# Kernel optimization log

Hardware: AMD Instinct MI355X
Metric: run time of the kernel (lower is better)

## Reference

```python
import jax, jax.numpy as jnp
import numpy as np

ALPHA = 0.2  # LeakyReLU negative slope


def setup_inputs() -> dict:
    key = jax.random.key(0)
    k1, k2, k3, k4 = jax.random.split(key, 4)
    N, IN, OUT = 8192, 512, 256
    x = jax.random.normal(k1, (N, IN), dtype=jnp.float32)
    adj = jnp.zeros((N, N), dtype=jnp.float32)  # accepted but unused by the module
    W = jax.random.normal(k2, (OUT, IN), dtype=jnp.float32) * (1.0 / np.sqrt(IN))
    a1 = jax.random.normal(k3, (OUT,), dtype=jnp.float32) * (1.0 / np.sqrt(OUT))
    a2 = jax.random.normal(k4, (OUT,), dtype=jnp.float32) * (1.0 / np.sqrt(OUT))
    return {"x": x, "adj": adj, "W": W, "a1": a1, "a2": a2}


def reference(x, adj, W, a1, a2):
    # h = tran(x): [N, OUT]
    h = x @ W.T
    # additive GAT scores: e[i, j] = a2 . h_i + a1 . h_j  (from unsqueeze(0)+unsqueeze(1))
    s1 = h @ a1  # [N], att1(h)
    s2 = h @ a2  # [N], att2(h)
    e = s2[:, None] + s1[None, :]  # [N, N]
    e = jnp.where(e > 0, e, ALPHA * e)  # LeakyReLU
    attn = jax.nn.softmax(e, axis=1)  # softmax over dim=1; dropout is identity in eval
    return attn @ h  # [N, OUT]
```

## Files before the change

### kernel.cpp

```cpp
#include <hip/hip_runtime.h>

#define NROW 8192
#define DIN  512
#define DOUT 256
#define NCHUNK 256
#define CLEN 32

constexpr size_t OFF_H      = 0;
constexpr size_t OFF_S1     = OFF_H + (size_t)NROW*DOUT*4;
constexpr size_t OFF_S2     = OFF_S1 + NROW*4;
constexpr size_t OFF_RANK   = OFF_S2 + NROW*4;
constexpr size_t OFF_MISC   = OFF_RANK + NROW*4;
constexpr size_t MEMSET_LEN = OFF_MISC + 256 - OFF_S1;
constexpr size_t OFF_S1S    = OFF_MISC + 256;
constexpr size_t OFF_PERM   = OFF_S1S + NROW*4;
constexpr size_t OFF_WHI    = OFF_PERM + NROW*4;
constexpr size_t OFF_WLO    = OFF_WHI + NROW*4;
constexpr size_t OFF_PRELOS = OFF_WLO + NROW*4;
constexpr size_t OFF_SUFHIS = OFF_PRELOS + 33024;
constexpr size_t OFF_CSLO   = OFF_SUFHIS + 33024;
constexpr size_t OFF_CSHI   = OFF_CSLO + 1024;
constexpr size_t OFF_TLO    = OFF_CSHI + 1024;
constexpr size_t OFF_THI    = OFF_TLO + (size_t)NCHUNK*DOUT*4;
constexpr size_t OFF_PRELO  = OFF_THI + (size_t)NCHUNK*DOUT*4;
constexpr size_t OFF_SUFHI  = OFF_PRELO + (size_t)(NROW+1)*DOUT*4;
constexpr size_t WS_NEED    = OFF_SUFHI + (size_t)(NROW+1)*DOUT*4;

typedef float f32x4 __attribute__((ext_vector_type(4)));
typedef short s16x8 __attribute__((ext_vector_type(8)));

__device__ __forceinline__ unsigned short bf16_rne(float f) {
  unsigned int u = __float_as_uint(f);
  return (unsigned short)((u + 0x7fffu + ((u >> 16) & 1u)) >> 16);
}
__device__ __forceinline__ unsigned short bf16_part(float f, bool lo) {
  unsigned short hi = bf16_rne(f);
  if (!lo) return hi;
  float r = f - __uint_as_float(((unsigned int)hi) << 16);
  return bf16_rne(r);
}
__device__ __forceinline__ s16x8 cvt8(const float4 u, const float4 v, bool lo) {
  s16x8 r;
  r[0] = (short)bf16_part(u.x, lo); r[1] = (short)bf16_part(u.y, lo);
  r[2] = (short)bf16_part(u.z, lo); r[3] = (short)bf16_part(u.w, lo);
  r[4] = (short)bf16_part(v.x, lo); r[5] = (short)bf16_part(v.y, lo);
  r[6] = (short)bf16_part(v.z, lo); r[7] = (short)bf16_part(v.w, lo);
  return r;
}

__global__ __launch_bounds__(256) void gemm_h_mfma(const float* __restrict__ x,
                                                   const float* __restrict__ W,
                                                   float* __restrict__ h) {
  __shared__ unsigned short As[64][40];
  __shared__ unsigned short Bs[64][40];
  const int tid = threadIdx.x;
  const int rowBase = blockIdx.x * 64;
  const int colBase = blockIdx.y * 64;
  const int wid = tid >> 6, lane = tid & 63;
  const int wRow = wid >> 1, wCol = wid & 1;
  const int lhi = lane >> 4, llo = lane & 15;

  f32x4 acc[2][2];
#pragma unroll
  for (int m = 0; m < 2; ++m)
#pragma unroll
    for (int n = 0; n < 2; ++n) acc[m][n] = (f32x4)(0.f);

  const int sr = tid >> 2;
  const int sq = tid & 3;
  const float* xsrc = x + (size_t)(rowBase + sr) * DIN + sq * 8;
  const float* wsrc = W + (size_t)(colBase + sr) * DIN + sq * 8;

  for (int pass = 0; pass < 3; ++pass) {
    const bool aLo = (pass == 1);
    const bool bLo = (pass == 2);
    for (int k0 = 0; k0 < DIN; k0 += 32) {
      float4 a0 = *(const float4*)(xsrc + k0);
      float4 a1v = *(const float4*)(xsrc + k0 + 4);
      float4 b0 = *(const float4*)(wsrc + k0);
      float4 b1 = *(const float4*)(wsrc + k0 + 4);
      s16x8 av = cvt8(a0, a1v, aLo);
      s16x8 bv = cvt8(b0, b1, bLo);
      __syncthreads();
      *(s16x8*)&As[sr][sq * 8] = av;
      *(s16x8*)&Bs[sr][sq * 8] = bv;
      __syncthreads();
      s16x8 af[2], bf[2];
#pragma unroll
      for (int m = 0; m < 2; ++m)
        af[m] = *(const s16x8*)&As[wRow * 32 + m * 16 + llo][lhi * 8];
#pragma unroll
      for (int n = 0; n < 2; ++n)
        bf[n] = *(const s16x8*)&Bs[wCol * 32 + n * 16 + llo][lhi * 8];
#pragma unroll
      for (int m = 0; m < 2; ++m)
#pragma unroll
        for (int n = 0; n < 2; ++n)
          acc[m][n] = __builtin_amdgcn_mfma_f32_16x16x32_bf16(af[m], bf[n], acc[m][n], 0, 0, 0);
    }
  }
#pragma unroll
  for (int m = 0; m < 2; ++m)
#pragma unroll
    for (int n = 0; n < 2; ++n) {
      const int col = colBase + wCol * 32 + n * 16 + llo;
#pragma unroll
      for (int j = 0; j < 4; ++j) {
        const int row = rowBase + wRow * 32 + m * 16 + lhi * 4 + j;
        h[(size_t)row * DOUT + col] = acc[m][n][j];
      }
    }
}

__global__ __launch_bounds__(256) void s1s2_rows(const float* __restrict__ h,
                                                 const float* __restrict__ a1,
                                                 const float* __restrict__ a2,
                                                 float* __restrict__ s1,
                                                 float* __restrict__ s2) {
  const int wid = threadIdx.x >> 6, lane = threadIdx.x & 63;
  const int row = blockIdx.x * 4 + wid;
  float4 hv = *(const float4*)(h + (size_t)row * DOUT + (lane << 2));
  float4 A1 = *(const float4*)(a1 + (lane << 2));
  float4 A2 = *(const float4*)(a2 + (lane << 2));
  float p1 = hv.x * A1.x + hv.y * A1.y + hv.z * A1.z + hv.w * A1.w;
  float p2 = hv.x * A2.x + hv.y * A2.y + hv.z * A2.z + hv.w * A2.w;
#pragma unroll
  for (int off = 32; off > 0; off >>= 1) {
    p1 += __shfl_xor(p1, off);
    p2 += __shfl_xor(p2, off);
  }
  if (lane == 0) { s1[row] = p1; s2[row] = p2; }
}

__global__ __launch_bounds__(256) void rank_count(const float* __restrict__ s1,
                                                  int* __restrict__ rank,
                                                  unsigned int* __restrict__ miscu) {
  __shared__ float sj[1024];
  __shared__ float wm[4];
  const int t = threadIdx.x;
  const int ib = blockIdx.x, jc = blockIdx.y;
  const int j0 = jc * 1024;
  *(float4*)&sj[t << 2] = *(const float4*)(s1 + j0 + (t << 2));
  const int i = ib * 256 + t;
  const float v = s1[i];
  __syncthreads();
  int cnt = 0;
#pragma unroll 4
  for (int q = 0; q < 256; ++q) {
    float4 sv = *(const float4*)&sj[q << 2];
    int jg = j0 + (q << 2);
    cnt += (int)(sv.x < v) + (int)((sv.x == v) & (jg + 0 < i));
    cnt += (int)(sv.y < v) + (int)((sv.y == v) & (jg + 1 < i));
    cnt += (int)(sv.z < v) + (int)((sv.z == v) & (jg + 2 < i));
    cnt += (int)(sv.w < v) + (int)((sv.w == v) & (jg + 3 < i));
  }
  atomicAdd(&rank[i], cnt);
  if (jc == 0) {
    float m = v;
#pragma unroll
    for (int off = 32; off > 0; off >>= 1) m = fmaxf(m, __shfl_down(m, off));
    if ((t & 63) == 0) wm[t >> 6] = m;
    __syncthreads();
    if (t == 0) {
      float mm = fmaxf(fmaxf(wm[0], wm[1]), fmaxf(wm[2], wm[3]));
      unsigned int b = __float_as_uint(mm);
      unsigned int enc = (b & 0x80000000u) ? ~b : (b | 0x80000000u);
      atomicMax(miscu, enc);
    }
  }
}

__global__ __launch_bounds__(256) void scatter_w(const float* __restrict__ s1,
                                                 const int* __restrict__ rank,
                                                 const unsigned int* __restrict__ miscu,
                                                 float* __restrict__ miscf,
                                                 float* __restrict__ s1s,
                                                 int* __restrict__ perm,
                                                 float* __restrict__ w_hi,
                                                 float* __restrict__ w_lo) {
  const int i = blockIdx.x * 256 + threadIdx.x;
  unsigned int e = miscu[0];
  unsigned int b = (e & 0x80000000u) ? (e & 0x7fffffffu) : ~e;
  const float M1 = __uint_as_float(b);
  const float v = s1[i];
  const int r = rank[i];
  s1s[r] = v;
  perm[r] = i;
  w_hi[r] = __expf(v - M1);
  w_lo[r] = __expf(0.2f * (v - M1));
  if (i == 0) miscf[0] = M1;
}

__global__ __launch_bounds__(256) void chunk_totals(const float* __restrict__ h,
                                                    const int* __restrict__ perm,
                                                    const float* __restrict__ w_hi,
                                                    const float* __restrict__ w_lo,
                                                    float* __restrict__ T_lo,
                                                    float* __restrict__ T_hi,
                                                    float* __restrict__ cs_lo,
                                                    float* __restrict__ cs_hi) {
  const int d = threadIdx.x, b = blockIdx.x;
  const int j0 = b * CLEN;
  float tlo = 0.f, thi = 0.f;
#pragma unroll
  for (int e = 0; e < CLEN; e += 4) {
    int4 p4 = *(const int4*)(perm + j0 + e);
    float4 wl4 = *(const float4*)(w_lo + j0 + e);
    float4 wh4 = *(const float4*)(w_hi + j0 + e);
    float h0 = h[(size_t)p4.x * DOUT + d];
    float h1 = h[(size_t)p4.y * DOUT + d];
    float h2 = h[(size_t)p4.z * DOUT + d];
    float h3 = h[(size_t)p4.w * DOUT + d];
    tlo += wl4.x * h0 + wl4.y * h1 + wl4.z * h2 + wl4.w * h3;
    thi += wh4.x * h0 + wh4.y * h1 + wh4.z * h2 + wh4.w * h3;
  }
  T_lo[b * DOUT + d] = tlo;
  T_hi[b * DOUT + d] = thi;
  if (d < 64) {
    float wl = (d < 32) ? w_lo[j0 + d] : 0.f;
    float wh = (d < 32) ? w_hi[j0 + d] : 0.f;
#pragma unroll
    for (int off = 32; off > 0; off >>= 1) {
      wl += __shfl_down(wl, off);
      wh += __shfl_down(wh, off);
    }
    if (d == 0) { cs_lo[b] = wl; cs_hi[b] = wh; }
  }
}

__global__ __launch_bounds__(256) void write_prefix(const float* __restrict__ h,
                                                    const int* __restrict__ perm,
                                                    const float* __restrict__ w_hi,
                                                    const float* __restrict__ w_lo,
                                                    const float* __restrict__ T_lo,
                                                    const float* __restrict__ T_hi,
                                                    const float* __restrict__ cs_lo,
                                                    const float* __restrict__ cs_hi,
                                                    float* __restrict__ PreLo,
                                                    float* __restrict__ SufHi,
                                                    float* __restrict__ prelo_s,
                                                    float* __restrict__ sufhi_s) {
  const int d = threadIdx.x, b = blockIdx.x;
  const int j0 = b * CLEN;
  if (d < 64) {
    float accp = 0.f, acct = 0.f;
    for (int p = d; p < NCHUNK; p += 64) {
      float cl = cs_lo[p], ch = cs_hi[p];
      accp += (p < b) ? cl : 0.f;
      acct += (p > b) ? ch : 0.f;
    }
#pragma unroll
    for (int off = 32; off > 0; off >>= 1) {
      accp += __shfl_down(accp, off);
      acct += __shfl_down(acct, off);
    }
    float pres  = __shfl(accp, 0);
    float tails = __shfl(acct, 0);
    float wl = (d < 32) ? w_lo[j0 + d] : 0.f;
    float wh = (d < 32) ? w_hi[j0 + d] : 0.f;
    float pl = wl, ph = wh;
#pragma unroll
    for (int off = 1; off < 32; off <<= 1) {
      float a = __shfl_up(pl, off);
      float c = __shfl_up(ph, off);
      if (d >= off) { pl += a; ph += c; }
    }
    float chunk_hi_tot = __shfl(ph, 31);
    if (d < 32) {
      prelo_s[j0 + d] = pres + (pl - wl);
      sufhi_s[j0 + d] = tails + (chunk_hi_tot - (ph - wh));
    }
    if (b == NCHUNK - 1 && d == 31) {
      prelo_s[NROW] = pres + pl;
      sufhi_s[NROW] = 0.f;
    }
  }
  float rl = 0.f, tail = 0.f;
#pragma unroll 8
  for (int p = 0; p < NCHUNK; ++p) {
    float vl = T_lo[p * DOUT + d];
    float vh = T_hi[p * DOUT + d];
    rl   += (p < b) ? vl : 0.f;
    tail += (p > b) ? vh : 0.f;
  }
  float hv[CLEN], wlv[CLEN], whv[CLEN];
  float ownHi = 0.f;
#pragma unroll
  for (int e = 0; e < CLEN; e += 4) {
    int4 p4 = *(const int4*)(perm + j0 + e);
    float4 wl4 = *(const float4*)(w_lo + j0 + e);
    float4 wh4 = *(const float4*)(w_hi + j0 + e);
    hv[e + 0] = h[(size_t)p4.x * DOUT + d];
    hv[e + 1] = h[(size_t)p4.y * DOUT + d];
    hv[e + 2] = h[(size_t)p4.z * DOUT + d];
    hv[e + 3] = h[(size_t)p4.w * DOUT + d];
    wlv[e + 0] = wl4.x; wlv[e + 1] = wl4.y; wlv[e + 2] = wl4.z; wlv[e + 3] = wl4.w;
    whv[e + 0] = wh4.x; whv[e + 1] = wh4.y; whv[e + 2] = wh4.z; whv[e + 3] = wh4.w;
    ownHi += wh4.x * hv[e] + wh4.y * hv[e + 1] + wh4.z * hv[e + 2] + wh4.w * hv[e + 3];
  }
  float shb = tail + ownHi;
  float preh = 0.f;
#pragma unroll
  for (int e = 0; e < CLEN; ++e) {
    size_t j = (size_t)(j0 + e);
    PreLo[j * DOUT + d] = rl;
    SufHi[j * DOUT + d] = shb - preh;
    rl   += wlv[e] * hv[e];
    preh += whv[e] * hv[e];
  }
  if (b == NCHUNK - 1) {
    PreLo[(size_t)NROW * DOUT + d] = rl;
    SufHi[(size_t)NROW * DOUT + d] = 0.f;
  }
}

__global__ __launch_bounds__(256) void finalize(const float* __restrict__ s2,
                                                const float* __restrict__ s1s,
                                                const float* __restrict__ miscf,
                                                const float* __restrict__ PreLo,
                                                const float* __restrict__ SufHi,
                                                const float* __restrict__ prelo_s,
                                                const float* __restrict__ sufhi_s,
                                                float* __restrict__ out) {
  const int wave = threadIdx.x >> 6, lane = threadIdx.x & 63;
  const int i = blockIdx.x * 4 + wave;
  const float c = s2[i];
  const float M1 = miscf[0];
  const float tval = -c;
  int lo = 0, hi = NROW;
  while (lo < hi) {
    int mid = (lo + hi) >> 1;
    if (s1s[mid] <= tval) lo = mid + 1; else hi = mid;
  }
  const int k = lo;
  const float u = c + M1;
  const float m = fmaxf(u, 0.2f * u);
  const float fh = __expf(u - m);
  const float fl = __expf(0.2f * u - m);
  const float den = fh * sufhi_s[k] + fl * prelo_s[k];
  const float inv = 1.f / den;
  float4 A = *(const float4*)(SufHi + (size_t)k * DOUT + (lane << 2));
  float4 B = *(const float4*)(PreLo + (size_t)k * DOUT + (lane << 2));
  float4 o;
  o.x = (fh * A.x + fl * B.x) * inv;
  o.y = (fh * A.y + fl * B.y) * inv;
  o.z = (fh * A.z + fl * B.z) * inv;
  o.w = (fh * A.w + fl * B.w) * inv;
  *(float4*)(out + (size_t)i * DOUT + (lane << 2)) = o;
}

extern "C" void kernel_launch(void* const* d_in, const int* in_sizes, int n_in,
                              void* d_out, int out_size, void* d_ws, size_t ws_size,
                              hipStream_t stream) {
  const float* x  = (const float*)d_in[0];
  const float* W  = (const float*)d_in[2];
  const float* a1 = (const float*)d_in[3];
  const float* a2 = (const float*)d_in[4];
  float* out = (float*)d_out;

  char* ws = (char*)d_ws;
  if (ws_size < WS_NEED) ws = (char*)d_in[1];

  float*        h       = (float*)(ws + OFF_H);
  float*        s1      = (float*)(ws + OFF_S1);
  float*        s2      = (float*)(ws + OFF_S2);
  int*          rank    = (int*)  (ws + OFF_RANK);
  unsigned int* miscu   = (unsigned int*)(ws + OFF_MISC);
  float*        miscf   = (float*)(ws + OFF_MISC) + 1;
  float*        s1s     = (float*)(ws + OFF_S1S);
  int*          perm    = (int*)  (ws + OFF_PERM);
  float*        w_hi    = (float*)(ws + OFF_WHI);
  float*        w_lo    = (float*)(ws + OFF_WLO);
  float*        prelo_s = (float*)(ws + OFF_PRELOS);
  float*        sufhi_s = (float*)(ws + OFF_SUFHIS);
  float*        cs_lo   = (float*)(ws + OFF_CSLO);
  float*        cs_hi   = (float*)(ws + OFF_CSHI);
  float*        T_lo    = (float*)(ws + OFF_TLO);
  float*        T_hi    = (float*)(ws + OFF_THI);
  float*        PreLo   = (float*)(ws + OFF_PRELO);
  float*        SufHi   = (float*)(ws + OFF_SUFHI);

  hipMemsetAsync(s1, 0, MEMSET_LEN, stream);

  gemm_h_mfma<<<dim3(NROW / 64, DOUT / 64), 256, 0, stream>>>(x, W, h);
  s1s2_rows<<<NROW / 4, 256, 0, stream>>>(h, a1, a2, s1, s2);
  rank_count<<<dim3(NROW / 256, 8), 256, 0, stream>>>(s1, rank, miscu);
  scatter_w<<<NROW / 256, 256, 0, stream>>>(s1, rank, miscu, miscf, s1s, perm, w_hi, w_lo);
  chunk_totals<<<NCHUNK, 256, 0, stream>>>(h, perm, w_hi, w_lo, T_lo, T_hi, cs_lo, cs_hi);
  write_prefix<<<NCHUNK, 256, 0, stream>>>(h, perm, w_hi, w_lo, T_lo, T_hi, cs_lo, cs_hi,
                                           PreLo, SufHi, prelo_s, sufhi_s);
  finalize<<<NROW / 4, 256, 0, stream>>>(s2, s1s, miscf, PreLo, SufHi, prelo_s, sufhi_s, out);
}
```

Before: 419.3 us.

## Pre-split inputs to bf16 hi/lo, single-pass 3-MFMA GEMM with fused score epilogue

A new kernel converts x and W once into bf16 high and low halves in workspace. The GEMM then streams those halves in a single K loop, issuing three MFMAs per tile instead of re-reading and re-converting the fp32 inputs over three passes. The next K tile is prefetched into registers. The s1/s2 dot products are folded into the GEMM epilogue with shuffles and atomicAdd, removing the separate row-reduction kernel. This adds an extra launch, more workspace traffic and LDS, and atomics whose float ordering is nondeterministic.

```diff
diff --git a/kernel.cpp b/kernel.cpp
--- a/kernel.cpp
+++ b/kernel.cpp
@@ -24,7 +24,11 @@
 constexpr size_t OFF_THI    = OFF_TLO + (size_t)NCHUNK*DOUT*4;
 constexpr size_t OFF_PRELO  = OFF_THI + (size_t)NCHUNK*DOUT*4;
 constexpr size_t OFF_SUFHI  = OFF_PRELO + (size_t)(NROW+1)*DOUT*4;
-constexpr size_t WS_NEED    = OFF_SUFHI + (size_t)(NROW+1)*DOUT*4;
+constexpr size_t OFF_XHI    = OFF_SUFHI + (size_t)(NROW+1)*DOUT*4;
+constexpr size_t OFF_XLO    = OFF_XHI + (size_t)NROW*DIN*2;
+constexpr size_t OFF_BHI    = OFF_XLO + (size_t)NROW*DIN*2;
+constexpr size_t OFF_BLO    = OFF_BHI + (size_t)DOUT*DIN*2;
+constexpr size_t WS_NEED    = OFF_BLO + (size_t)DOUT*DIN*2;
 
 typedef float f32x4 __attribute__((ext_vector_type(4)));
 typedef short s16x8 __attribute__((ext_vector_type(8)));
@@ -33,26 +37,49 @@
   unsigned int u = __float_as_uint(f);
   return (unsigned short)((u + 0x7fffu + ((u >> 16) & 1u)) >> 16);
 }
-__device__ __forceinline__ unsigned short bf16_part(float f, bool lo) {
-  unsigned short hi = bf16_rne(f);
-  if (!lo) return hi;
-  float r = f - __uint_as_float(((unsigned int)hi) << 16);
-  return bf16_rne(r);
-}
-__device__ __forceinline__ s16x8 cvt8(const float4 u, const float4 v, bool lo) {
-  s16x8 r;
-  r[0] = (short)bf16_part(u.x, lo); r[1] = (short)bf16_part(u.y, lo);
-  r[2] = (short)bf16_part(u.z, lo); r[3] = (short)bf16_part(u.w, lo);
-  r[4] = (short)bf16_part(v.x, lo); r[5] = (short)bf16_part(v.y, lo);
-  r[6] = (short)bf16_part(v.z, lo); r[7] = (short)bf16_part(v.w, lo);
-  return r;
-}
-
-__global__ __launch_bounds__(256) void gemm_h_mfma(const float* __restrict__ x,
-                                                   const float* __restrict__ W,
-                                                   float* __restrict__ h) {
-  __shared__ unsigned short As[64][40];
-  __shared__ unsigned short Bs[64][40];
+
+__global__ __launch_bounds__(256) void split_inputs(const float* __restrict__ x,
+                                                    const float* __restrict__ W,
+                                                    unsigned short* __restrict__ Xhi,
+                                                    unsigned short* __restrict__ Xlo,
+                                                    unsigned short* __restrict__ Bhi,
+                                                    unsigned short* __restrict__ Blo) {
+  const int b = blockIdx.x;
+  const float* src;
+  unsigned short *dh, *dl;
+  size_t off;
+  if (b < 2048) {
+    off = ((size_t)b * 256 + threadIdx.x) * 8;
+    src = x; dh = Xhi; dl = Xlo;
+  } else {
+    off = ((size_t)(b - 2048) * 256 + threadIdx.x) * 8;
+    src = W; dh = Bhi; dl = Blo;
+  }
+  float4 u = *(const float4*)(src + off);
+  float4 v = *(const float4*)(src + off + 4);
+  float f[8] = {u.x, u.y, u.z, u.w, v.x, v.y, v.z, v.w};
+  s16x8 hv, lv;
+#pragma unroll
+  for (int j = 0; j < 8; ++j) {
+    unsigned short hh = bf16_rne(f[j]);
+    float r = f[j] - __uint_as_float(((unsigned int)hh) << 16);
+    hv[j] = (short)hh;
+    lv[j] = (short)bf16_rne(r);
+  }
+  *(s16x8*)(dh + off) = hv;
+  *(s16x8*)(dl + off) = lv;
+}
+
+__global__ __launch_bounds__(256) void gemm_h_mfma(const unsigned short* __restrict__ Xhi,
+                                                   const unsigned short* __restrict__ Xlo,
+                                                   const unsigned short* __restrict__ Bhi,
+                                                   const unsigned short* __restrict__ Blo,
+                                                   const float* __restrict__ a1,
+                                                   const float* __restrict__ a2,
+                                                   float* __restrict__ h,
+                                                   float* __restrict__ s1,
+                                                   float* __restrict__ s2) {
+  __shared__ unsigned short AsH[64][40], AsL[64][40], BsH[64][40], BsL[64][40];
   const int tid = threadIdx.x;
   const int rowBase = blockIdx.x * 64;
   const int colBase = blockIdx.y * 64;
@@ -68,39 +95,59 @@
 
   const int sr = tid >> 2;
   const int sq = tid & 3;
-  const float* xsrc = x + (size_t)(rowBase + sr) * DIN + sq * 8;
-  const float* wsrc = W + (size_t)(colBase + sr) * DIN + sq * 8;
-
-  for (int pass = 0; pass < 3; ++pass) {
-    const bool aLo = (pass == 1);
-    const bool bLo = (pass == 2);
-    for (int k0 = 0; k0 < DIN; k0 += 32) {
-      float4 a0 = *(const float4*)(xsrc + k0);
-      float4 a1v = *(const float4*)(xsrc + k0 + 4);
-      float4 b0 = *(const float4*)(wsrc + k0);
-      float4 b1 = *(const float4*)(wsrc + k0 + 4);
-      s16x8 av = cvt8(a0, a1v, aLo);
-      s16x8 bv = cvt8(b0, b1, bLo);
-      __syncthreads();
-      *(s16x8*)&As[sr][sq * 8] = av;
-      *(s16x8*)&Bs[sr][sq * 8] = bv;
-      __syncthreads();
-      s16x8 af[2], bf[2];
-#pragma unroll
-      for (int m = 0; m < 2; ++m)
-        af[m] = *(const s16x8*)&As[wRow * 32 + m * 16 + llo][lhi * 8];
-#pragma unroll
-      for (int n = 0; n < 2; ++n)
-        bf[n] = *(const s16x8*)&Bs[wCol * 32 + n * 16 + llo][lhi * 8];
-#pragma unroll
-      for (int m = 0; m < 2; ++m)
-#pragma unroll
-        for (int n = 0; n < 2; ++n)
-          acc[m][n] = __builtin_amdgcn_mfma_f32_16x16x32_bf16(af[m], bf[n], acc[m][n], 0, 0, 0);
-    }
-  }
-#pragma unroll
-  for (int m = 0; m < 2; ++m)
+  const unsigned short* xh = Xhi + (size_t)(rowBase + sr) * DIN + sq * 8;
+  const unsigned short* xl = Xlo + (size_t)(rowBase + sr) * DIN + sq * 8;
+  const unsigned short* bh = Bhi + (size_t)(colBase + sr) * DIN + sq * 8;
+  const unsigned short* bl = Blo + (size_t)(colBase + sr) * DIN + sq * 8;
+
+  s16x8 rah = *(const s16x8*)(xh);
+  s16x8 ral = *(const s16x8*)(xl);
+  s16x8 rbh = *(const s16x8*)(bh);
+  s16x8 rbl = *(const s16x8*)(bl);
+
+  for (int k0 = 0; k0 < DIN; k0 += 32) {
+    __syncthreads();
+    *(s16x8*)&AsH[sr][sq * 8] = rah;
+    *(s16x8*)&AsL[sr][sq * 8] = ral;
+    *(s16x8*)&BsH[sr][sq * 8] = rbh;
+    *(s16x8*)&BsL[sr][sq * 8] = rbl;
+    __syncthreads();
+    if (k0 + 32 < DIN) {
+      rah = *(const s16x8*)(xh + k0 + 32);
+      ral = *(const s16x8*)(xl + k0 + 32);
+      rbh = *(const s16x8*)(bh + k0 + 32);
+      rbl = *(const s16x8*)(bl + k0 + 32);
+    }
+    s16x8 afh[2], afl[2], bfh[2], bfl[2];
+#pragma unroll
+    for (int m = 0; m < 2; ++m) {
+      afh[m] = *(const s16x8*)&AsH[wRow * 32 + m * 16 + llo][lhi * 8];
+      afl[m] = *(const s16x8*)&AsL[wRow * 32 + m * 16 + llo][lhi * 8];
+    }
+#pragma unroll
+    for (int n = 0; n < 2; ++n) {
+      bfh[n] = *(const s16x8*)&BsH[wCol * 32 + n * 16 + llo][lhi * 8];
+      bfl[n] = *(const s16x8*)&BsL[wCol * 32 + n * 16 + llo][lhi * 8];
+    }
+#pragma unroll
+    for (int m = 0; m < 2; ++m)
+#pragma unroll
+      for (int n = 0; n < 2; ++n) {
+        acc[m][n] = __builtin_amdgcn_mfma_f32_16x16x32_bf16(afh[m], bfh[n], acc[m][n], 0, 0, 0);
+        acc[m][n] = __builtin_amdgcn_mfma_f32_16x16x32_bf16(afl[m], bfh[n], acc[m][n], 0, 0, 0);
+        acc[m][n] = __builtin_amdgcn_mfma_f32_16x16x32_bf16(afh[m], bfl[n], acc[m][n], 0, 0, 0);
+      }
+  }
+  float a1c[2], a2c[2];
+#pragma unroll
+  for (int n = 0; n < 2; ++n) {
+    const int col = colBase + wCol * 32 + n * 16 + llo;
+    a1c[n] = a1[col];
+    a2c[n] = a2[col];
+  }
+#pragma unroll
+  for (int m = 0; m < 2; ++m) {
+    float p1[4] = {0.f, 0.f, 0.f, 0.f}, p2[4] = {0.f, 0.f, 0.f, 0.f};
 #pragma unroll
     for (int n = 0; n < 2; ++n) {
       const int col = colBase + wCol * 32 + n * 16 + llo;
@@ -108,28 +155,27 @@
       for (int j = 0; j < 4; ++j) {
         const int row = rowBase + wRow * 32 + m * 16 + lhi * 4 + j;
         h[(size_t)row * DOUT + col] = acc[m][n][j];
+        p1[j] = fmaf(acc[m][n][j], a1c[n], p1[j]);
+        p2[j] = fmaf(acc[m][n][j], a2c[n], p2[j]);
       }
     }
-}
-
-__global__ __launch_bounds__(256) void s1s2_rows(const float* __restrict__ h,
-                                                 const float* __restrict__ a1,
-                                                 const float* __restrict__ a2,
-                                                 float* __restrict__ s1,
-                                                 float* __restrict__ s2) {
-  const int wid = threadIdx.x >> 6, lane = threadIdx.x & 63;
-  const int row = blockIdx.x * 4 + wid;
-  float4 hv = *(const float4*)(h + (size_t)row * DOUT + (lane << 2));
-  float4 A1 = *(const float4*)(a1 + (lane << 2));
-  float4 A2 = *(const float4*)(a2 + (lane << 2));
-  float p1 = hv.x * A1.x + hv.y * A1.y + hv.z * A1.z + hv.w * A1.w;
-  float p2 = hv.x * A2.x + hv.y * A2.y + hv.z * A2.z + hv.w * A2.w;
-#pragma unroll
-  for (int off = 32; off > 0; off >>= 1) {
-    p1 += __shfl_xor(p1, off);
-    p2 += __shfl_xor(p2, off);
-  }
-  if (lane == 0) { s1[row] = p1; s2[row] = p2; }
+#pragma unroll
+    for (int j = 0; j < 4; ++j) {
+#pragma unroll
+      for (int msk = 1; msk < 16; msk <<= 1) {
+        p1[j] += __shfl_xor(p1[j], msk);
+        p2[j] += __shfl_xor(p2[j], msk);
+      }
+    }
+    if (llo == 0) {
+#pragma unroll
+      for (int j = 0; j < 4; ++j) {
+        const int row = rowBase + wRow * 32 + m * 16 + lhi * 4 + j;
+        atomicAdd(&s1[row], p1[j]);
+        atomicAdd(&s2[row], p2[j]);
+      }
+    }
+  }
 }
 
 __global__ __launch_bounds__(256) void rank_count(const float* __restrict__ s1,
@@ -361,29 +407,34 @@
   char* ws = (char*)d_ws;
   if (ws_size < WS_NEED) ws = (char*)d_in[1];
 
-  float*        h       = (float*)(ws + OFF_H);
-  float*        s1      = (float*)(ws + OFF_S1);
-  float*        s2      = (float*)(ws + OFF_S2);
-  int*          rank    = (int*)  (ws + OFF_RANK);
-  unsigned int* miscu   = (unsigned int*)(ws + OFF_MISC);
-  float*        miscf   = (float*)(ws + OFF_MISC) + 1;
-  float*        s1s     = (float*)(ws + OFF_S1S);
-  int*          perm    = (int*)  (ws + OFF_PERM);
-  float*        w_hi    = (float*)(ws + OFF_WHI);
-  float*        w_lo    = (float*)(ws + OFF_WLO);
-  float*        prelo_s = (float*)(ws + OFF_PRELOS);
-  float*        sufhi_s = (float*)(ws + OFF_SUFHIS);
-  float*        cs_lo   = (float*)(ws + OFF_CSLO);
-  float*        cs_hi   = (float*)(ws + OFF_CSHI);
-  float*        T_lo    = (float*)(ws + OFF_TLO);
-  float*        T_hi    = (float*)(ws + OFF_THI);
-  float*        PreLo   = (float*)(ws + OFF_PRELO);
-  float*        SufHi   = (float*)(ws + OFF_SUFHI);
+  float*          h       = (float*)(ws + OFF_H);
+  float*          s1      = (float*)(ws + OFF_S1);
+  float*          s2      = (float*)(ws + OFF_S2);
+  int*            rank    = (int*)  (ws + OFF_RANK);
+  unsigned int*   miscu   = (unsigned int*)(ws + OFF_MISC);
+  float*          miscf   = (float*)(ws + OFF_MISC) + 1;
+  float*          s1s     = (float*)(ws + OFF_S1S);
+  int*            perm    = (int*)  (ws + OFF_PERM);
+  float*          w_hi    = (float*)(ws + OFF_WHI);
+  float*          w_lo    = (float*)(ws + OFF_WLO);
+  float*          prelo_s = (float*)(ws + OFF_PRELOS);
+  float*          sufhi_s = (float*)(ws + OFF_SUFHIS);
+  float*          cs_lo   = (float*)(ws + OFF_CSLO);
+  float*          cs_hi   = (float*)(ws + OFF_CSHI);
+  float*          T_lo    = (float*)(ws + OFF_TLO);
+  float*          T_hi    = (float*)(ws + OFF_THI);
+  float*          PreLo   = (float*)(ws + OFF_PRELO);
+  float*          SufHi   = (float*)(ws + OFF_SUFHI);
+  unsigned short* Xhi     = (unsigned short*)(ws + OFF_XHI);
+  unsigned short* Xlo     = (unsigned short*)(ws + OFF_XLO);
+  unsigned short* Bhi     = (unsigned short*)(ws + OFF_BHI);
+  unsigned short* Blo     = (unsigned short*)(ws + OFF_BLO);
 
   hipMemsetAsync(s1, 0, MEMSET_LEN, stream);
 
-  gemm_h_mfma<<<dim3(NROW / 64, DOUT / 64), 256, 0, stream>>>(x, W, h);
-  s1s2_rows<<<NROW / 4, 256, 0, stream>>>(h, a1, a2, s1, s2);
+  split_inputs<<<2048 + 64, 256, 0, stream>>>(x, W, Xhi, Xlo, Bhi, Blo);
+  gemm_h_mfma<<<dim3(NROW / 64, DOUT / 64), 256, 0, stream>>>(Xhi, Xlo, Bhi, Blo,
+                                                              a1, a2, h, s1, s2);
   rank_count<<<dim3(NROW / 256, 8), 256, 0, stream>>>(s1, rank, miscu);
   scatter_w<<<NROW / 256, 256, 0, stream>>>(s1, rank, miscu, miscf, s1s, perm, w_hi, w_lo);
   chunk_totals<<<NCHUNK, 256, 0, stream>>>(h, perm, w_hi, w_lo, T_lo, T_hi, cs_lo, cs_hi);
```

New measurement: 381.0 us. 9.2% less time.
